# Optimization experiments

Hardware: AMD Instinct MI355X
Metric: run time of the kernel (lower is better)

## Reference

```python
import jax, jax.numpy as jnp
import numpy as np

N, C, L = 64, 3, 4096
K, S = 128, 64  # num_shapelets, shapelets_size


def setup_inputs() -> dict:
    key = jax.random.key(0)
    kx, ks = jax.random.split(key)
    x = jax.random.normal(kx, (N, C, L), dtype=jnp.float32)
    shapelets = jax.random.normal(ks, (C, K, S), dtype=jnp.float32)
    return {"x": x, "shapelets": shapelets}


def _min_euclid(x, shapelets):
    # x: (N, C, L); shapelets: (C, K, S)
    # Torch does unfold -> cdist -> min over windows -> min over channels.
    # We compute ||x_w - s||^2 = ||x_w||^2 + ||s||^2 - 2<x_w, s> with sliding
    # dot products via grouped 1-D conv (avoids materializing the unfold).
    C_, K_, S_ = shapelets.shape
    n = x.shape[0]
    filt = shapelets.reshape(C_ * K_, 1, S_)  # OIW, grouped by channel
    dots = jax.lax.conv_general_dilated(
        x, filt, window_strides=(1,), padding="VALID",
        dimension_numbers=("NCW", "OIW", "NCW"),
        feature_group_count=C_)                      # (N, C*K, W)
    ones = jnp.ones((C_, 1, S_), x.dtype)
    x2 = jax.lax.conv_general_dilated(
        x * x, ones, window_strides=(1,), padding="VALID",
        dimension_numbers=("NCW", "OIW", "NCW"),
        feature_group_count=C_)                      # (N, C, W) sliding ||x_w||^2
    W_ = dots.shape[-1]
    dots = dots.reshape(n, C_, K_, W_)               # (N, C, K, W)
    s2 = jnp.sum(shapelets * shapelets, axis=-1)     # (C, K)
    d2 = x2[:, :, None, :] + s2[None, :, :, None] - 2.0 * dots
    d = jnp.sqrt(jnp.maximum(d2, 0.0))               # Euclidean distance (N,C,K,W)
    d = jnp.min(d, axis=3)                           # min over windows -> (N, C, K)
    d = jnp.min(d, axis=1)                           # min over channels -> (N, K)
    return d[:, None, :]                             # (N, 1, K)


def reference(x, shapelets):
    return _min_euclid(x, shapelets)
```

## Files before the change

kernel.cpp:

```cpp
#include <hip/hip_runtime.h>
#include <hip/hip_bf16.h>

#define NN 64
#define CC 3
#define LL 4096
#define SS 64
#define KK 128
#define WW 4033
#define BLKN 8

typedef __attribute__((ext_vector_type(8))) short v8s;
typedef __attribute__((ext_vector_type(4))) float v4f;

#define WS_CNT_OFF 32768
#define WS_HS2_OFF 33024

__device__ __forceinline__ unsigned bf16_rne(float f) {
    unsigned u = __float_as_uint(f);
    return (u + 0x7FFFu + ((u >> 16) & 1u)) >> 16;
}

__global__ __launch_bounds__(256) void me_init(
        const float* __restrict__ shp,
        unsigned* __restrict__ d2g,
        unsigned* __restrict__ cnt,
        float* __restrict__ hs2g) {
    int tid = blockIdx.x * 256 + threadIdx.x;
    uint4 inf4 = {0x7F800000u, 0x7F800000u, 0x7F800000u, 0x7F800000u};
    ((uint4*)d2g)[tid] = inf4;
    if (tid < NN) cnt[tid] = 0u;
    if (tid < CC * KK) {
        const float* r = shp + tid * SS;
        float a = 0.f;
        #pragma unroll 8
        for (int s = 0; s < SS; ++s) a += r[s] * r[s];
        hs2g[tid] = -0.5f * a;
    }
}

__global__ __launch_bounds__(256, 2) void me_main(
        const float* __restrict__ x,
        const float* __restrict__ shp,
        const float* __restrict__ hs2g,
        unsigned* __restrict__ d2g,
        unsigned* __restrict__ cnt,
        float* __restrict__ out) {

    __shared__ __align__(16) ushort shb[CC * 8192];
    __shared__ __align__(8) ushort xs2[2][CC][640];
    __shared__ float Pp[CC][580];
    __shared__ float hx2s[CC][512];
    __shared__ unsigned red[KK];
    __shared__ int lastflag;

    const int b    = blockIdx.x;
    const int n    = b >> 3;
    const int tg   = b & 7;
    const int w0   = tg * 512;
    const int t    = threadIdx.x;
    const int lane = t & 63, wave = t >> 6;
    const int quad = lane >> 4, col = lane & 15;
    const int wbase = wave * 128;

    if (t < KK) red[t] = 0x7F800000u;

    #pragma unroll
    for (int it = 0; it < 12; ++it) {
        int cidx = t + it * 256;
        int c   = cidx >> 10;
        int r   = cidx & 1023;
        int nt  = r >> 7;
        int scb = (r >> 6) & 1;
        int l   = r & 63;
        int row  = nt * 16 + (l & 15);
        int koff = scb * 32 + (l >> 4) * 8;
        const float* s = shp + (size_t)(c * KK + row) * SS + koff;
        float4 f0 = *(const float4*)s;
        float4 f1 = *(const float4*)(s + 4);
        uint4 o;
        o.x = (bf16_rne(f0.y) << 16) | bf16_rne(f0.x);
        o.y = (bf16_rne(f0.w) << 16) | bf16_rne(f0.z);
        o.z = (bf16_rne(f1.y) << 16) | bf16_rne(f1.x);
        o.w = (bf16_rne(f1.w) << 16) | bf16_rne(f1.z);
        ((uint4*)shb)[cidx] = o;
    }

    float hsv[CC][8];
    #pragma unroll
    for (int c = 0; c < CC; ++c)
        #pragma unroll
        for (int nt = 0; nt < 8; ++nt)
            hsv[c][nt] = hs2g[c * KK + nt * 16 + col];

    const float* xb = x + (size_t)n * (CC * LL);

    if (wave < 3) {
        const float* xc = xb + wave * LL;
        float carry = 0.f;
        #pragma unroll
        for (int seg = 0; seg < 9; ++seg) {
            int idx = seg * 64 + lane;
            int gi  = w0 + idx;
            float v = (gi < LL) ? xc[gi] : 0.f;
            ushort hv = (ushort)bf16_rne(v);
            xs2[0][wave][idx] = hv;
            if (idx > 0) xs2[1][wave][idx - 1] = hv;
            float sq = v * v;
            #pragma unroll
            for (int d = 1; d < 64; d <<= 1) {
                float u = __shfl_up(sq, d, 64);
                if (lane >= d) sq += u;
            }
            sq += carry;
            Pp[wave][idx] = sq;
            carry = __shfl(sq, 63, 64);
        }
    }
    __syncthreads();

    #pragma unroll
    for (int it = 0; it < 6; ++it) {
        int e = t + it * 256;
        int c = e >> 9, w = e & 511;
        float I1 = Pp[c][w + 63];
        float I0 = (w > 0) ? Pp[c][w - 1] : 0.f;
        hx2s[c][w] = (w0 + w < WW) ? (-0.5f * (I1 - I0)) : -1e30f;
    }
    __syncthreads();

    float rmax[8];
    #pragma unroll
    for (int nt = 0; nt < 8; ++nt) rmax[nt] = -3.4e38f;

    #pragma unroll
    for (int c = 0; c < CC; ++c) {
        v4f hxv[8];
        #pragma unroll
        for (int mt = 0; mt < 8; ++mt)
            hxv[mt] = *(const v4f*)(&hx2s[c][wbase + mt * 16 + quad * 4]);
        v8s af[8][2];
        #pragma unroll
        for (int mt = 0; mt < 8; ++mt)
            #pragma unroll
            for (int sc = 0; sc < 2; ++sc) {
                int e0 = wbase + mt * 16 + col + sc * 32 + quad * 8;
                int p  = col & 1;
                const uint* ap = (const uint*)&xs2[p][c][e0 - p];
                union { v8s v; uint u[4]; } au;
                au.u[0] = ap[0]; au.u[1] = ap[1];
                au.u[2] = ap[2]; au.u[3] = ap[3];
                af[mt][sc] = au.v;
            }
        #pragma unroll
        for (int g = 0; g < 4; ++g) {
            v4f acc[2][8];
            #pragma unroll
            for (int nt2 = 0; nt2 < 2; ++nt2) {
                float h = hsv[c][g * 2 + nt2];
                v4f a = {h, h, h, h};
                #pragma unroll
                for (int mt = 0; mt < 8; ++mt) acc[nt2][mt] = a;
            }
            #pragma unroll
            for (int sc = 0; sc < 2; ++sc)
                #pragma unroll
                for (int nt2 = 0; nt2 < 2; ++nt2) {
                    int nt = g * 2 + nt2;
                    v8s bfr = *(const v8s*)(shb + (((c * 8 + nt) * 2 + sc) * 64 + lane) * 8);
                    #pragma unroll
                    for (int mt = 0; mt < 8; ++mt)
                        acc[nt2][mt] = __builtin_amdgcn_mfma_f32_16x16x32_bf16(
                            af[mt][sc], bfr, acc[nt2][mt], 0, 0, 0);
                }
            #pragma unroll
            for (int nt2 = 0; nt2 < 2; ++nt2) {
                float m = -3.4e38f;
                #pragma unroll
                for (int mt = 0; mt < 8; ++mt) {
                    v4f a = acc[nt2][mt];
                    #pragma unroll
                    for (int r = 0; r < 4; ++r)
                        m = fmaxf(m, a[r] + hxv[mt][r]);
                }
                rmax[g * 2 + nt2] = fmaxf(rmax[g * 2 + nt2], m);
            }
        }
    }

    #pragma unroll
    for (int nt = 0; nt < 8; ++nt) {
        float v = rmax[nt];
        v = fmaxf(v, __shfl_xor(v, 16, 64));
        v = fmaxf(v, __shfl_xor(v, 32, 64));
        rmax[nt] = v;
    }
    if (quad == 0) {
        #pragma unroll
        for (int nt = 0; nt < 8; ++nt) {
            float d2 = fmaxf(-2.f * rmax[nt], 0.f);
            atomicMin(&red[nt * 16 + col], __float_as_uint(d2));
        }
    }
    __syncthreads();
    if (t < KK) atomicMin(&d2g[n * KK + t], red[t]);

    __syncthreads();
    if (t == 0) {
        unsigned old = atomicAdd(&cnt[n], 1u);
        lastflag = (old == BLKN - 1) ? 1 : 0;
    }
    __syncthreads();
    if (lastflag && t < KK) {
        unsigned bits = atomicMin(&d2g[n * KK + t], 0x7F800000u);
        out[n * KK + t] = sqrtf(__uint_as_float(bits));
    }
}

extern "C" void kernel_launch(void* const* d_in, const int* in_sizes, int n_in,
                              void* d_out, int out_size, void* d_ws, size_t ws_size,
                              hipStream_t stream) {
    const float* x   = (const float*)d_in[0];
    const float* shp = (const float*)d_in[1];
    unsigned* d2g  = (unsigned*)d_ws;
    unsigned* cnt  = (unsigned*)((char*)d_ws + WS_CNT_OFF);
    float*    hs2g = (float*)((char*)d_ws + WS_HS2_OFF);
    float* out = (float*)d_out;

    hipLaunchKernelGGL(me_init, dim3(8), dim3(256), 0, stream, shp, d2g, cnt, hs2g);
    hipLaunchKernelGGL(me_main, dim3(NN * BLKN), dim3(256), 0, stream,
                       x, shp, hs2g, d2g, cnt, out);
}
```

Baseline: 77.68 us.

## Use 4 shifted bf16 copies for aligned A loads, register prefix sums, fold x2 into accumulator init

Stores four shifted copies of the bf16 input so each MFMA A-fragment can be read with 8-byte aligned loads instead of four 4-byte loads. The window squared-norm term is now computed from register prefix sums with shuffles, which removes the Pp shared buffer and one block barrier. The hx2 bias is folded into the accumulator initialisation, so the epilogue only takes a max. The cost is extra LDS writes and footprint for the shifted copies, plus more adds at accumulator init.

```diff
diff --git a/kernel.cpp b/kernel.cpp
--- a/kernel.cpp
+++ b/kernel.cpp
@@ -47,8 +47,7 @@
         float* __restrict__ out) {
 
     __shared__ __align__(16) ushort shb[CC * 8192];
-    __shared__ __align__(8) ushort xs2[2][CC][640];
-    __shared__ float Pp[CC][580];
+    __shared__ __align__(16) ushort xs4[4][CC][640];
     __shared__ float hx2s[CC][512];
     __shared__ unsigned red[KK];
     __shared__ int lastflag;
@@ -96,6 +95,8 @@
 
     if (wave < 3) {
         const float* xc = xb + wave * LL;
+        float P[9];
+        float ca[9];
         float carry = 0.f;
         #pragma unroll
         for (int seg = 0; seg < 9; ++seg) {
@@ -103,8 +104,9 @@
             int gi  = w0 + idx;
             float v = (gi < LL) ? xc[gi] : 0.f;
             ushort hv = (ushort)bf16_rne(v);
-            xs2[0][wave][idx] = hv;
-            if (idx > 0) xs2[1][wave][idx - 1] = hv;
+            #pragma unroll
+            for (int s = 0; s < 4; ++s)
+                if (idx >= s) xs4[s][wave][idx - s] = hv;
             float sq = v * v;
             #pragma unroll
             for (int d = 1; d < 64; d <<= 1) {
@@ -112,19 +114,20 @@
                 if (lane >= d) sq += u;
             }
             sq += carry;
-            Pp[wave][idx] = sq;
+            P[seg] = sq;
             carry = __shfl(sq, 63, 64);
-        }
-    }
-    __syncthreads();
-
-    #pragma unroll
-    for (int it = 0; it < 6; ++it) {
-        int e = t + it * 256;
-        int c = e >> 9, w = e & 511;
-        float I1 = Pp[c][w + 63];
-        float I0 = (w > 0) ? Pp[c][w - 1] : 0.f;
-        hx2s[c][w] = (w0 + w < WW) ? (-0.5f * (I1 - I0)) : -1e30f;
+            ca[seg] = carry;
+        }
+        #pragma unroll
+        for (int seg = 0; seg < 8; ++seg) {
+            float i1s = __shfl_up(P[seg + 1], 1, 64);
+            float i0s = __shfl_up(P[seg], 1, 64);
+            float prevca = seg ? ca[seg - 1] : 0.f;
+            float I1 = (lane == 0) ? ca[seg] : i1s;
+            float I0 = (lane == 0) ? prevca : i0s;
+            int idx = seg * 64 + lane;
+            hx2s[wave][idx] = (w0 + idx < WW) ? (-0.5f * (I1 - I0)) : -1e30f;
+        }
     }
     __syncthreads();
 
@@ -144,11 +147,12 @@
             #pragma unroll
             for (int sc = 0; sc < 2; ++sc) {
                 int e0 = wbase + mt * 16 + col + sc * 32 + quad * 8;
-                int p  = col & 1;
-                const uint* ap = (const uint*)&xs2[p][c][e0 - p];
+                int p  = col & 3;
+                const uint2* ap = (const uint2*)&xs4[p][c][e0 - p];
+                uint2 a01 = ap[0], a23 = ap[1];
                 union { v8s v; uint u[4]; } au;
-                au.u[0] = ap[0]; au.u[1] = ap[1];
-                au.u[2] = ap[2]; au.u[3] = ap[3];
+                au.u[0] = a01.x; au.u[1] = a01.y;
+                au.u[2] = a23.x; au.u[3] = a23.y;
                 af[mt][sc] = au.v;
             }
         #pragma unroll
@@ -157,9 +161,13 @@
             #pragma unroll
             for (int nt2 = 0; nt2 < 2; ++nt2) {
                 float h = hsv[c][g * 2 + nt2];
-                v4f a = {h, h, h, h};
                 #pragma unroll
-                for (int mt = 0; mt < 8; ++mt) acc[nt2][mt] = a;
+                for (int mt = 0; mt < 8; ++mt) {
+                    v4f a;
+                    a[0] = h + hxv[mt][0]; a[1] = h + hxv[mt][1];
+                    a[2] = h + hxv[mt][2]; a[3] = h + hxv[mt][3];
+                    acc[nt2][mt] = a;
+                }
             }
             #pragma unroll
             for (int sc = 0; sc < 2; ++sc)
@@ -178,9 +186,7 @@
                 #pragma unroll
                 for (int mt = 0; mt < 8; ++mt) {
                     v4f a = acc[nt2][mt];
-                    #pragma unroll
-                    for (int r = 0; r < 4; ++r)
-                        m = fmaxf(m, a[r] + hxv[mt][r]);
+                    m = fmaxf(m, fmaxf(fmaxf(a[0], a[1]), fmaxf(a[2], a[3])));
                 }
                 rmax[g * 2 + nt2] = fmaxf(rmax[g * 2 + nt2], m);
             }
```

Result: slower. 79.43 us (+2.3%).
